# Optimization experiments

Measured on AMD Instinct MI355X. Metric: run time of the kernel, lower is better.

The kernel has to match this reference:

```python
import jax, jax.numpy as jnp
import numpy as np

N, E = 50000, 800000
DIN, DOUT, DEDGE, HEADS = 128, 128, 64, 1


def setup_inputs() -> dict:
    key = jax.random.key(0)
    ks = jax.random.split(key, 16)
    s = 0.02
    inp = {
        "x": jax.random.normal(ks[0], (N, DIN), jnp.float32),
        "edge_index": jax.random.randint(ks[1], (2, E), 0, N, dtype=jnp.int32),
        "edge_attr": jax.random.normal(ks[2], (E, DEDGE), jnp.float32),
        # TransformerConv params (PyG defaults: q/k/v/skip have bias, lin_edge has no bias)
        "Wq": jax.random.normal(ks[3], (DIN, HEADS * DOUT), jnp.float32) * s,
        "bq": jnp.zeros((HEADS * DOUT,), jnp.float32),
        "Wk": jax.random.normal(ks[4], (DIN, HEADS * DOUT), jnp.float32) * s,
        "bk": jnp.zeros((HEADS * DOUT,), jnp.float32),
        "Wv": jax.random.normal(ks[5], (DIN, HEADS * DOUT), jnp.float32) * s,
        "bv": jnp.zeros((HEADS * DOUT,), jnp.float32),
        "We": jax.random.normal(ks[6], (DEDGE, HEADS * DOUT), jnp.float32) * s,
        "Wskip": jax.random.normal(ks[7], (DIN, HEADS * DOUT), jnp.float32) * s,
        "bskip": jnp.zeros((HEADS * DOUT,), jnp.float32),
        # LayerNorm
        "ln_g": jnp.ones((DOUT,), jnp.float32),
        "ln_b": jnp.zeros((DOUT,), jnp.float32),
        # GatedResidualConnection
        "Wres": jax.random.normal(ks[8], (DIN, DOUT), jnp.float32) * s,
        "bres": jnp.zeros((DOUT,), jnp.float32),
        "Wgate": jax.random.normal(ks[9], (DIN, 1), jnp.float32) * s,
        "bgate": jnp.zeros((1,), jnp.float32),
    }
    return inp


def _transformer_conv(x, edge_index, edge_attr, Wq, bq, Wk, bk, Wv, bv, We, Wskip, bskip):
    H, C = HEADS, DOUT
    src, dst = edge_index[0], edge_index[1]  # j -> i (aggregate at dst)
    q = (x @ Wq + bq).reshape(-1, H, C)
    k = (x @ Wk + bk).reshape(-1, H, C)
    v = (x @ Wv + bv).reshape(-1, H, C)
    e = (edge_attr @ We).reshape(-1, H, C)  # [E,H,C]
    k_j = k[src] + e
    v_j = v[src] + e
    q_i = q[dst]
    alpha = jnp.sum(q_i * k_j, axis=-1) / jnp.sqrt(jnp.float32(C))  # [E,H]
    # segment softmax over incoming edges of each dst node
    amax = jax.ops.segment_max(alpha, dst, num_segments=N)  # [N,H]
    ex = jnp.exp(alpha - amax[dst])
    denom = jax.ops.segment_sum(ex, dst, num_segments=N)  # [N,H]
    p = ex / denom[dst]  # [E,H]
    out = jax.ops.segment_sum(p[..., None] * v_j, dst, num_segments=N)  # [N,H,C]
    out = out.reshape(-1, H * C)
    out = out + (x @ Wskip + bskip)  # root weight skip
    return out


def reference(x, edge_index, edge_attr, Wq, bq, Wk, bk, Wv, bv, We, Wskip, bskip,
              ln_g, ln_b, Wres, bres, Wgate, bgate):
    out = _transformer_conv(x, edge_index, edge_attr, Wq, bq, Wk, bk, Wv, bv, We, Wskip, bskip)
    # LayerNorm(out_channels)
    mu = jnp.mean(out, axis=-1, keepdims=True)
    var = jnp.mean(jnp.square(out - mu), axis=-1, keepdims=True)
    out = (out - mu) / jnp.sqrt(var + 1e-5) * ln_g + ln_b
    out = jax.nn.relu(out)
    # gated residual
    residual = x @ Wres + bres
    gate = jax.nn.sigmoid(x @ Wgate + bgate)  # [N,1]
    return gate * out + (1.0 - gate) * residual
```

## Files before the change

kernel.cpp:

```cpp
#include <hip/hip_runtime.h>
#include <math.h>

#define NN 50000
#define EE 800000
#define NPAD 50048
#define PC 768

typedef short bf16x8 __attribute__((ext_vector_type(8)));
typedef float f32x4 __attribute__((ext_vector_type(4)));

#define ASCALE 0.08838834764831845f

__device__ inline unsigned short f2bf(float f)
{
    unsigned u = __float_as_uint(f);
    u = u + 0x7fff + ((u >> 16) & 1);
    return (unsigned short)(u >> 16);
}

__global__ __launch_bounds__(256) void k_wprep(const float* __restrict__ Wq,
                                               const float* __restrict__ bq,
                                               const float* __restrict__ We,
                                               float* __restrict__ wqe,
                                               float* __restrict__ bqe)
{
    int idx = blockIdx.x * 256 + threadIdx.x;
    if (idx < 8192) {
        int r = idx >> 6, m = idx & 63;
        float acc = 0.f;
        for (int c = 0; c < 128; ++c) acc += Wq[r * 128 + c] * We[m * 128 + c];
        wqe[r * 64 + m] = acc;
    } else if (idx < 8256) {
        int m = idx - 8192;
        float acc = 0.f;
        for (int c = 0; c < 128; ++c) acc += bq[c] * We[m * 128 + c];
        bqe[m] = acc;
    }
}

__global__ __launch_bounds__(256) void k_packx(const float* __restrict__ x,
                                               short* __restrict__ Xb)
{
    int t = blockIdx.x * 256 + threadIdx.x;
    int base = t * 4;
    if (base >= NPAD * 128) return;
    short s0 = 0, s1 = 0, s2 = 0, s3 = 0;
    if (base < NN * 128) {
        const float4 v = *(const float4*)(x + base);
        s0 = f2bf(v.x); s1 = f2bf(v.y); s2 = f2bf(v.z); s3 = f2bf(v.w);
    }
    short4 o; o.x = s0; o.y = s1; o.z = s2; o.w = s3;
    *(short4*)(Xb + base) = o;
}

__global__ __launch_bounds__(256) void k_packw(
    const float* __restrict__ Wq, const float* __restrict__ bq,
    const float* __restrict__ Wk, const float* __restrict__ bk,
    const float* __restrict__ Wv, const float* __restrict__ bv,
    const float* __restrict__ Wskip, const float* __restrict__ bskip,
    const float* __restrict__ Wres, const float* __restrict__ bres,
    const float* __restrict__ Wgate, const float* __restrict__ bgate,
    const float* __restrict__ wqe, const float* __restrict__ bqe,
    const float* __restrict__ We,
    short* __restrict__ WT, float* __restrict__ bias,
    unsigned short* __restrict__ WeTb)
{
    int idx = blockIdx.x * 256 + threadIdx.x;
    if (idx < PC * 128) {
        int col = idx >> 7, k = idx & 127;
        float v;
        if (col < 128)      v = Wq[k * 128 + col];
        else if (col < 256) v = Wk[k * 128 + (col - 128)];
        else if (col < 384) v = Wv[k * 128 + (col - 256)];
        else if (col < 512) v = Wskip[k * 128 + (col - 384)];
        else if (col < 640) v = Wres[k * 128 + (col - 512)];
        else if (col < 704) v = wqe[k * 64 + (col - 640)];
        else if (col == 704) v = Wgate[k];
        else                v = 0.f;
        WT[col * 128 + k] = (short)f2bf(v);
    } else if (idx < PC * 128 + PC) {
        int col = idx - PC * 128;
        float b;
        if (col < 128)      b = bq[col];
        else if (col < 256) b = bk[col - 128];
        else if (col < 384) b = bv[col - 256];
        else if (col < 512) b = bskip[col - 384];
        else if (col < 640) b = bres[col - 512];
        else if (col < 704) b = bqe[col - 640];
        else if (col == 704) b = bgate[0];
        else                b = 0.f;
        bias[col] = b;
    } else if (idx < PC * 128 + PC + 128 * 72) {
        int i2 = idx - (PC * 128 + PC);
        int c = i2 / 72, kk = i2 % 72;
        WeTb[i2] = (kk < 64) ? f2bf(We[kk * 128 + c]) : (unsigned short)0;
    }
}

#define LROW 136
__global__ __launch_bounds__(256) void k_gemm(const short* __restrict__ Xb,
                                              const short* __restrict__ WT,
                                              const float* __restrict__ bias,
                                              float* __restrict__ P,
                                              unsigned short* __restrict__ KVb16)
{
    __shared__ short Al[128 * LROW];
    __shared__ short Bl[64 * LROW];

    int bn = blockIdx.x;
    int bm = blockIdx.y;
    int tid = threadIdx.x;

    const short* gA = Xb + (size_t)bm * 128 * 128;
    const short* gB = WT + (size_t)bn * 64 * 128;

#pragma unroll
    for (int it = 0; it < 8; ++it) {
        int g = it * 256 + tid;
        int row = g >> 4, c8 = g & 15;
        *(bf16x8*)&Al[row * LROW + c8 * 8] = *(const bf16x8*)(gA + g * 8);
    }
#pragma unroll
    for (int it = 0; it < 4; ++it) {
        int g = it * 256 + tid;
        int row = g >> 4, c8 = g & 15;
        *(bf16x8*)&Bl[row * LROW + c8 * 8] = *(const bf16x8*)(gB + g * 8);
    }
    __syncthreads();

    int wave = tid >> 6, lane = tid & 63;
    int quad = lane >> 4, l16 = lane & 15;
    int r0 = wave * 32;

    f32x4 acc[2][4] = {};
#pragma unroll
    for (int ks = 0; ks < 4; ++ks) {
        int k0 = ks * 32 + quad * 8;
        bf16x8 af0 = *(const bf16x8*)&Al[(r0 + l16) * LROW + k0];
        bf16x8 af1 = *(const bf16x8*)&Al[(r0 + 16 + l16) * LROW + k0];
#pragma unroll
        for (int cn = 0; cn < 4; ++cn) {
            bf16x8 bfr = *(const bf16x8*)&Bl[(cn * 16 + l16) * LROW + k0];
            acc[0][cn] = __builtin_amdgcn_mfma_f32_16x16x32_bf16(af0, bfr, acc[0][cn], 0, 0, 0);
            acc[1][cn] = __builtin_amdgcn_mfma_f32_16x16x32_bf16(af1, bfr, acc[1][cn], 0, 0, 0);
        }
    }

    bool isKV = (bn >= 2 && bn <= 5);
#pragma unroll
    for (int half = 0; half < 2; ++half) {
        int growb = bm * 128 + r0 + half * 16 + quad * 4;
#pragma unroll
        for (int cn = 0; cn < 4; ++cn) {
            int gcol = bn * 64 + cn * 16 + l16;
            float b = bias[gcol];
#pragma unroll
            for (int i = 0; i < 4; ++i) {
                int grow = growb + i;
                if (grow < NN) {
                    float v = acc[half][cn][i] + b;
                    if (isKV) {
                        int c, sub;
                        if (gcol < 192)      { c = gcol - 128; sub = 0; }
                        else if (gcol < 256) { c = gcol - 192; sub = 1; }
                        else if (gcol < 320) { c = gcol - 256; sub = 2; }
                        else                 { c = gcol - 320; sub = 3; }
                        KVb16[(size_t)grow * 256 + c * 4 + sub] = f2bf(v);
                    } else {
                        if (gcol == 704) v = 1.f / (1.f + __expf(-v));
                        P[(size_t)grow * PC + gcol] = v;
                    }
                }
            }
        }
    }
}

__global__ __launch_bounds__(256) void k_hist(const int* __restrict__ ei,
                                              int* __restrict__ deg, int E)
{
    int e = blockIdx.x * 256 + threadIdx.x;
    if (e < E) atomicAdd(&deg[ei[E + e]], 1);
}

__global__ __launch_bounds__(256) void k_scan1(const int* __restrict__ deg,
                                               int* __restrict__ rs,
                                               int* __restrict__ cs, int n)
{
    __shared__ int sh[256];
    int base = blockIdx.x * 1024;
    int t = threadIdx.x;
    int idx = base + t * 4;
    int v[4];
#pragma unroll
    for (int k = 0; k < 4; ++k) v[k] = (idx + k < n) ? deg[idx + k] : 0;
    int sum = v[0] + v[1] + v[2] + v[3];
    sh[t] = sum;
    __syncthreads();
    for (int off = 1; off < 256; off <<= 1) {
        int add = (t >= off) ? sh[t - off] : 0;
        __syncthreads();
        sh[t] += add;
        __syncthreads();
    }
    int run = sh[t] - sum;
    if (t == 255) cs[blockIdx.x] = sh[255];
#pragma unroll
    for (int k = 0; k < 4; ++k) {
        if (idx + k < n) rs[idx + k] = run;
        run += v[k];
    }
}

__global__ void k_scan2(int* __restrict__ cs, int nc)
{
    __shared__ int sh[64];
    int t = threadIdx.x;
    sh[t] = (t < nc) ? cs[t] : 0;
    __syncthreads();
    if (t == 0) {
        int acc = 0;
        for (int i = 0; i < nc; ++i) { int v = sh[i]; sh[i] = acc; acc += v; }
    }
    __syncthreads();
    if (t < nc) cs[t] = sh[t];
}

__global__ __launch_bounds__(256) void k_scan3(int* __restrict__ rs,
                                               const int* __restrict__ cs,
                                               int* __restrict__ cur, int n, int E)
{
    int i = blockIdx.x * 256 + threadIdx.x;
    if (i < n) {
        int v = rs[i] + cs[i >> 10];
        rs[i] = v;
        cur[i] = v;
    } else if (i == n) {
        rs[n] = E;
    }
}

__global__ __launch_bounds__(256) void k_scatter(const int* __restrict__ ei,
                                                 int* __restrict__ cur,
                                                 int2* __restrict__ sj, int E)
{
    int e = blockIdx.x * 256 + threadIdx.x;
    if (e < E) {
        int d = ei[E + e];
        int pos = atomicAdd(&cur[d], 1);
        int2 v; v.x = ei[e]; v.y = e;
        sj[pos] = v;
    }
}

__global__ __launch_bounds__(256) void k_attn_fused(
    const float* __restrict__ P, const unsigned int* __restrict__ KVb,
    const float* __restrict__ ea, const unsigned short* __restrict__ WeTb,
    const int* __restrict__ rs, const int2* __restrict__ sj,
    const float* __restrict__ ln_g, const float* __restrict__ ln_b,
    float* __restrict__ out)
{
    __shared__ unsigned short Sb_l[4 * 64];
    __shared__ float att_l[4 * 128];

    int tid = threadIdx.x;
    int wave = tid >> 6, lane = tid & 63;
    int node = blockIdx.x * 4 + wave;

    const float* Prow = P + (size_t)node * PC;
    float q0 = Prow[lane];
    float q1 = Prow[64 + lane];
    float wq = Prow[640 + lane];

    float accd = 0.f, t0 = 0.f, t1 = 0.f, sA = 0.f;
    int beg = rs[node], end = rs[node + 1];

    int p = beg;
    for (; p + 8 <= end; p += 8) {
        float pp[8], aa[8], v0[8], v1[8];
#pragma unroll
        for (int u = 0; u < 8; ++u) {
            long long sv = __builtin_nontemporal_load((const long long*)(sj + p + u));
            int sx = (int)sv, sy = (int)(sv >> 32);
            uint2 kv2 = *(const uint2*)(KVb + (size_t)sx * 128 + 2 * lane);
            float a = __builtin_nontemporal_load(ea + (size_t)sy * 64 + lane);
            float k0 = __uint_as_float(kv2.x << 16);
            float k1 = __uint_as_float(kv2.x & 0xffff0000u);
            v0[u] = __uint_as_float(kv2.y << 16);
            v1[u] = __uint_as_float(kv2.y & 0xffff0000u);
            aa[u] = a;
            pp[u] = q0 * k0 + q1 * k1 + wq * a;
        }
#pragma unroll
        for (int o = 32; o > 0; o >>= 1) {
#pragma unroll
            for (int u = 0; u < 8; ++u) pp[u] += __shfl_xor(pp[u], o);
        }
#pragma unroll
        for (int u = 0; u < 8; ++u) {
            float ex = __expf(pp[u] * ASCALE);
            accd += ex;
            t0 += ex * v0[u];
            t1 += ex * v1[u];
            sA += ex * aa[u];
        }
    }
    for (; p + 4 <= end; p += 4) {
        float pp[4], aa[4], v0[4], v1[4];
#pragma unroll
        for (int u = 0; u < 4; ++u) {
            long long sv = __builtin_nontemporal_load((const long long*)(sj + p + u));
            int sx = (int)sv, sy = (int)(sv >> 32);
            uint2 kv2 = *(const uint2*)(KVb + (size_t)sx * 128 + 2 * lane);
            float a = __builtin_nontemporal_load(ea + (size_t)sy * 64 + lane);
            float k0 = __uint_as_float(kv2.x << 16);
            float k1 = __uint_as_float(kv2.x & 0xffff0000u);
            v0[u] = __uint_as_float(kv2.y << 16);
            v1[u] = __uint_as_float(kv2.y & 0xffff0000u);
            aa[u] = a;
            pp[u] = q0 * k0 + q1 * k1 + wq * a;
        }
#pragma unroll
        for (int o = 32; o > 0; o >>= 1) {
#pragma unroll
            for (int u = 0; u < 4; ++u) pp[u] += __shfl_xor(pp[u], o);
        }
#pragma unroll
        for (int u = 0; u < 4; ++u) {
            float ex = __expf(pp[u] * ASCALE);
            accd += ex;
            t0 += ex * v0[u];
            t1 += ex * v1[u];
            sA += ex * aa[u];
        }
    }
    for (; p < end; ++p) {
        long long sv = __builtin_nontemporal_load((const long long*)(sj + p));
        int sx = (int)sv, sy = (int)(sv >> 32);
        uint2 kv2 = *(const uint2*)(KVb + (size_t)sx * 128 + 2 * lane);
        float a = __builtin_nontemporal_load(ea + (size_t)sy * 64 + lane);
        float k0 = __uint_as_float(kv2.x << 16);
        float k1 = __uint_as_float(kv2.x & 0xffff0000u);
        float vv0 = __uint_as_float(kv2.y << 16);
        float vv1 = __uint_as_float(kv2.y & 0xffff0000u);
        float part = q0 * k0 + q1 * k1 + wq * a;
#pragma unroll
        for (int o = 32; o > 0; o >>= 1) part += __shfl_xor(part, o);
        float ex = __expf(part * ASCALE);
        accd += ex;
        t0 += ex * vv0;
        t1 += ex * vv1;
        sA += ex * a;
    }


    Sb_l[wave * 64 + lane] = f2bf(sA);
    __syncthreads();

    {
        int quad = lane >> 4, l16 = lane & 15;
        int arow = l16 & 3;
        bf16x8 a0 = *(const bf16x8*)&Sb_l[arow * 64 + quad * 8];
        bf16x8 a1 = *(const bf16x8*)&Sb_l[arow * 64 + 32 + quad * 8];
#pragma unroll
        for (int c2 = 0; c2 < 2; ++c2) {
            int cn = wave * 2 + c2;
            int r = cn * 16 + l16;
            bf16x8 b0 = *(const bf16x8*)(WeTb + r * 72 + quad * 8);
            bf16x8 b1 = *(const bf16x8*)(WeTb + r * 72 + 32 + quad * 8);
            f32x4 acc = {};
            acc = __builtin_amdgcn_mfma_f32_16x16x32_bf16(a0, b0, acc, 0, 0, 0);
            acc = __builtin_amdgcn_mfma_f32_16x16x32_bf16(a1, b1, acc, 0, 0, 0);
            if (quad == 0) {
#pragma unroll
                for (int i = 0; i < 4; ++i)
                    att_l[i * 128 + cn * 16 + l16] = acc[i];
            }
        }
    }
    __syncthreads();

    float rcp = accd > 0.f ? 1.f / accd : 0.f;
    float a0f = (t0 + att_l[wave * 128 + lane]) * rcp + Prow[384 + lane];
    float a1f = (t1 + att_l[wave * 128 + 64 + lane]) * rcp + Prow[448 + lane];

    float s = a0f + a1f;
#pragma unroll
    for (int o = 32; o > 0; o >>= 1) s += __shfl_xor(s, o);
    float mean = s * (1.f / 128.f);
    float d0 = a0f - mean, d1 = a1f - mean;
    float vs = d0 * d0 + d1 * d1;
#pragma unroll
    for (int o = 32; o > 0; o >>= 1) vs += __shfl_xor(vs, o);
    float inv = rsqrtf(vs * (1.f / 128.f) + 1e-5f);
    float n0 = d0 * inv * ln_g[lane] + ln_b[lane];
    float n1 = d1 * inv * ln_g[64 + lane] + ln_b[64 + lane];
    n0 = fmaxf(n0, 0.f);
    n1 = fmaxf(n1, 0.f);

    float g = Prow[704];
    float r0 = Prow[512 + lane];
    float r1 = Prow[576 + lane];
    out[(size_t)node * 128 + lane] = g * n0 + (1.f - g) * r0;
    out[(size_t)node * 128 + 64 + lane] = g * n1 + (1.f - g) * r1;
}

extern "C" void kernel_launch(void* const* d_in, const int* in_sizes, int n_in,
                              void* d_out, int out_size, void* d_ws, size_t ws_size,
                              hipStream_t stream)
{
    const float* x     = (const float*)d_in[0];
    const int*   ei    = (const int*)d_in[1];
    const float* ea    = (const float*)d_in[2];
    const float* Wq    = (const float*)d_in[3];
    const float* bq    = (const float*)d_in[4];
    const float* Wk    = (const float*)d_in[5];
    const float* bk    = (const float*)d_in[6];
    const float* Wv    = (const float*)d_in[7];
    const float* bv    = (const float*)d_in[8];
    const float* We    = (const float*)d_in[9];
    const float* Wskip = (const float*)d_in[10];
    const float* bskip = (const float*)d_in[11];
    const float* ln_g  = (const float*)d_in[12];
    const float* ln_b  = (const float*)d_in[13];
    const float* Wres  = (const float*)d_in[14];
    const float* bres  = (const float*)d_in[15];
    const float* Wgate = (const float*)d_in[16];
    const float* bgate = (const float*)d_in[17];
    float* out = (float*)d_out;

    float* W = (float*)d_ws;
    size_t o = 0;
    auto falloc = [&](size_t e) { size_t r = o; o += e; return r; };
    size_t oP    = falloc((size_t)NN * PC);
    size_t oWQE  = falloc(8192);
    size_t oBQE  = falloc(64);
    size_t oBIAS = falloc(PC);
    size_t oKVB  = falloc((size_t)NN * 128);

    short* SB = (short*)(W + o);
    size_t oXB  = 0;
    size_t oWT  = oXB + (size_t)NPAD * 128;
    size_t oWET = oWT + (size_t)PC * 128;
    size_t sh_total = oWET + 128 * 72;

    int* IB = (int*)(SB + ((sh_total + 1) & ~(size_t)1));
    size_t io = 0;
    auto ialloc = [&](size_t e) { size_t r = io; io += e; return r; };
    size_t oSJ   = ialloc((size_t)2 * EE);
    size_t oDEG  = ialloc(NN);
    size_t oRS   = ialloc(NN + 1);
    size_t oCUR  = ialloc(NN);
    size_t oCS   = ialloc(64);

    hipMemsetAsync(IB + oDEG, 0, NN * sizeof(int), stream);

    k_wprep<<<33, 256, 0, stream>>>(Wq, bq, We, W + oWQE, W + oBQE);
    k_packx<<<(NPAD * 128 / 4 + 255) / 256, 256, 0, stream>>>(x, SB + oXB);
    k_packw<<<(PC * 128 + PC + 128 * 72 + 255) / 256, 256, 0, stream>>>(
        Wq, bq, Wk, bk, Wv, bv, Wskip, bskip, Wres, bres, Wgate, bgate,
        W + oWQE, W + oBQE, We, SB + oWT, W + oBIAS,
        (unsigned short*)(SB + oWET));

    dim3 ggrid(PC / 64, NPAD / 128);
    k_gemm<<<ggrid, 256, 0, stream>>>(SB + oXB, SB + oWT, W + oBIAS, W + oP,
                                      (unsigned short*)(W + oKVB));

    k_hist<<<(EE + 255) / 256, 256, 0, stream>>>(ei, IB + oDEG, EE);
    k_scan1<<<49, 256, 0, stream>>>(IB + oDEG, IB + oRS, IB + oCS, NN);
    k_scan2<<<1, 64, 0, stream>>>(IB + oCS, 49);
    k_scan3<<<(NN + 256) / 256, 256, 0, stream>>>(IB + oRS, IB + oCS, IB + oCUR, NN, EE);
    k_scatter<<<(EE + 255) / 256, 256, 0, stream>>>(ei, IB + oCUR, (int2*)(IB + oSJ), EE);

    k_attn_fused<<<NN / 4, 256, 0, stream>>>(
        W + oP, (const unsigned int*)(W + oKVB), ea,
        (const unsigned short*)(SB + oWET),
        IB + oRS, (const int2*)(IB + oSJ), ln_g, ln_b, out);
}
```

Baseline: 565.3 us.

## Store skip/residual/gate projections in bf16 and schedule nodes by degree

The GEMM output is split into an fp32 query buffer and a bf16 buffer holding the skip, residual, qe and gate columns, which shrinks the per-node projection traffic written by the GEMM and read by the attention kernel. A counting sort by in-degree (histogram, scan, scatter) builds a node permutation so the waves in a block handle nodes with similar degree, reducing load imbalance inside blocks. This adds three small kernels, and the bf16 rounding of the skip and residual terms slightly lowers precision.

```diff
diff --git a/kernel.cpp b/kernel.cpp
--- a/kernel.cpp
+++ b/kernel.cpp
@@ -16,6 +16,11 @@
     unsigned u = __float_as_uint(f);
     u = u + 0x7fff + ((u >> 16) & 1);
     return (unsigned short)(u >> 16);
+}
+
+__device__ inline float bfu(unsigned short us)
+{
+    return __uint_as_float((unsigned)us << 16);
 }
 
 __global__ __launch_bounds__(256) void k_wprep(const float* __restrict__ Wq,
@@ -101,7 +106,8 @@
 __global__ __launch_bounds__(256) void k_gemm(const short* __restrict__ Xb,
                                               const short* __restrict__ WT,
                                               const float* __restrict__ bias,
-                                              float* __restrict__ P,
+                                              float* __restrict__ Pq,
+                                              unsigned short* __restrict__ Pe,
                                               unsigned short* __restrict__ KVb16)
 {
     __shared__ short Al[128 * LROW];
@@ -159,16 +165,18 @@
                 int grow = growb + i;
                 if (grow < NN) {
                     float v = acc[half][cn][i] + b;
-                    if (isKV) {
+                    if (bn < 2) {
+                        Pq[(size_t)grow * 128 + gcol] = v;
+                    } else if (isKV) {
                         int c, sub;
                         if (gcol < 192)      { c = gcol - 128; sub = 0; }
                         else if (gcol < 256) { c = gcol - 192; sub = 1; }
                         else if (gcol < 320) { c = gcol - 256; sub = 2; }
                         else                 { c = gcol - 320; sub = 3; }
                         KVb16[(size_t)grow * 256 + c * 4 + sub] = f2bf(v);
-                    } else {
+                    } else if (gcol <= 704) {
                         if (gcol == 704) v = 1.f / (1.f + __expf(-v));
-                        P[(size_t)grow * PC + gcol] = v;
+                        Pe[(size_t)grow * 384 + (gcol - 384)] = f2bf(v);
                     }
                 }
             }
@@ -253,10 +261,48 @@
     }
 }
 
+__global__ __launch_bounds__(256) void k_dhist(const int* __restrict__ deg,
+                                               int* __restrict__ dcnt)
+{
+    int i = blockIdx.x * 256 + threadIdx.x;
+    if (i < NN) {
+        int d = deg[i]; if (d > 63) d = 63;
+        atomicAdd(&dcnt[d], 1);
+    }
+}
+
+__global__ void k_dscan(const int* __restrict__ dcnt, int* __restrict__ dcur)
+{
+    __shared__ int sh[64];
+    int t = threadIdx.x;
+    sh[t] = dcnt[t];
+    __syncthreads();
+    if (t == 0) {
+        int acc = 0;
+        for (int d = 63; d >= 0; --d) { int v = sh[d]; sh[d] = acc; acc += v; }
+    }
+    __syncthreads();
+    dcur[t] = sh[t];
+}
+
+__global__ __launch_bounds__(256) void k_dscatter(const int* __restrict__ deg,
+                                                  int* __restrict__ dcur,
+                                                  int* __restrict__ perm)
+{
+    int i = blockIdx.x * 256 + threadIdx.x;
+    if (i < NN) {
+        int d = deg[i]; if (d > 63) d = 63;
+        int pos = atomicAdd(&dcur[d], 1);
+        perm[pos] = i;
+    }
+}
+
 __global__ __launch_bounds__(256) void k_attn_fused(
-    const float* __restrict__ P, const unsigned int* __restrict__ KVb,
+    const float* __restrict__ Pq, const unsigned short* __restrict__ Pe,
+    const unsigned int* __restrict__ KVb,
     const float* __restrict__ ea, const unsigned short* __restrict__ WeTb,
     const int* __restrict__ rs, const int2* __restrict__ sj,
+    const int* __restrict__ perm,
     const float* __restrict__ ln_g, const float* __restrict__ ln_b,
     float* __restrict__ out)
 {
@@ -265,12 +311,13 @@
 
     int tid = threadIdx.x;
     int wave = tid >> 6, lane = tid & 63;
-    int node = blockIdx.x * 4 + wave;
-
-    const float* Prow = P + (size_t)node * PC;
-    float q0 = Prow[lane];
-    float q1 = Prow[64 + lane];
-    float wq = Prow[640 + lane];
+    int node = perm[blockIdx.x * 4 + wave];
+
+    const float* Qrow = Pq + (size_t)node * 128;
+    const unsigned short* Erow = Pe + (size_t)node * 384;
+    float q0 = Qrow[lane];
+    float q1 = Qrow[64 + lane];
+    float wq = bfu(Erow[256 + lane]);
 
     float accd = 0.f, t0 = 0.f, t1 = 0.f, sA = 0.f;
     int beg = rs[node], end = rs[node + 1];
@@ -381,8 +428,8 @@
     __syncthreads();
 
     float rcp = accd > 0.f ? 1.f / accd : 0.f;
-    float a0f = (t0 + att_l[wave * 128 + lane]) * rcp + Prow[384 + lane];
-    float a1f = (t1 + att_l[wave * 128 + 64 + lane]) * rcp + Prow[448 + lane];
+    float a0f = (t0 + att_l[wave * 128 + lane]) * rcp + bfu(Erow[lane]);
+    float a1f = (t1 + att_l[wave * 128 + 64 + lane]) * rcp + bfu(Erow[64 + lane]);
 
     float s = a0f + a1f;
 #pragma unroll
@@ -398,9 +445,9 @@
     n0 = fmaxf(n0, 0.f);
     n1 = fmaxf(n1, 0.f);
 
-    float g = Prow[704];
-    float r0 = Prow[512 + lane];
-    float r1 = Prow[576 + lane];
+    float g = bfu(Erow[320]);
+    float r0 = bfu(Erow[128 + lane]);
+    float r1 = bfu(Erow[192 + lane]);
     out[(size_t)node * 128 + lane] = g * n0 + (1.f - g) * r0;
     out[(size_t)node * 128 + 64 + lane] = g * n1 + (1.f - g) * r1;
 }
@@ -432,7 +479,7 @@
     float* W = (float*)d_ws;
     size_t o = 0;
     auto falloc = [&](size_t e) { size_t r = o; o += e; return r; };
-    size_t oP    = falloc((size_t)NN * PC);
+    size_t oPQ   = falloc((size_t)NN * 128);
     size_t oWQE  = falloc(8192);
     size_t oBQE  = falloc(64);
     size_t oBIAS = falloc(PC);
@@ -442,18 +489,22 @@
     size_t oXB  = 0;
     size_t oWT  = oXB + (size_t)NPAD * 128;
     size_t oWET = oWT + (size_t)PC * 128;
-    size_t sh_total = oWET + 128 * 72;
+    size_t oPE  = oWET + 128 * 72;
+    size_t sh_total = oPE + (size_t)NN * 384;
 
     int* IB = (int*)(SB + ((sh_total + 1) & ~(size_t)1));
     size_t io = 0;
     auto ialloc = [&](size_t e) { size_t r = io; io += e; return r; };
     size_t oSJ   = ialloc((size_t)2 * EE);
     size_t oDEG  = ialloc(NN);
+    size_t oDCNT = ialloc(64);
     size_t oRS   = ialloc(NN + 1);
     size_t oCUR  = ialloc(NN);
     size_t oCS   = ialloc(64);
-
-    hipMemsetAsync(IB + oDEG, 0, NN * sizeof(int), stream);
+    size_t oDCUR = ialloc(64);
+    size_t oPERM = ialloc(NN);
+
+    hipMemsetAsync(IB + oDEG, 0, (NN + 64) * sizeof(int), stream);
 
     k_wprep<<<33, 256, 0, stream>>>(Wq, bq, We, W + oWQE, W + oBQE);
     k_packx<<<(NPAD * 128 / 4 + 255) / 256, 256, 0, stream>>>(x, SB + oXB);
@@ -463,17 +514,22 @@
         (unsigned short*)(SB + oWET));
 
     dim3 ggrid(PC / 64, NPAD / 128);
-    k_gemm<<<ggrid, 256, 0, stream>>>(SB + oXB, SB + oWT, W + oBIAS, W + oP,
+    k_gemm<<<ggrid, 256, 0, stream>>>(SB + oXB, SB + oWT, W + oBIAS, W + oPQ,
+                                      (unsigned short*)(SB + oPE),
                                       (unsigned short*)(W + oKVB));
 
     k_hist<<<(EE + 255) / 256, 256, 0, stream>>>(ei, IB + oDEG, EE);
+    k_dhist<<<(NN + 255) / 256, 256, 0, stream>>>(IB + oDEG, IB + oDCNT);
     k_scan1<<<49, 256, 0, stream>>>(IB + oDEG, IB + oRS, IB + oCS, NN);
     k_scan2<<<1, 64, 0, stream>>>(IB + oCS, 49);
     k_scan3<<<(NN + 256) / 256, 256, 0, stream>>>(IB + oRS, IB + oCS, IB + oCUR, NN, EE);
+    k_dscan<<<1, 64, 0, stream>>>(IB + oDCNT, IB + oDCUR);
     k_scatter<<<(EE + 255) / 256, 256, 0, stream>>>(ei, IB + oCUR, (int2*)(IB + oSJ), EE);
+    k_dscatter<<<(NN + 255) / 256, 256, 0, stream>>>(IB + oDEG, IB + oDCUR, IB + oPERM);
 
     k_attn_fused<<<NN / 4, 256, 0, stream>>>(
-        W + oP, (const unsigned int*)(W + oKVB), ea,
+        W + oPQ, (const unsigned short*)(SB + oPE),
+        (const unsigned int*)(W + oKVB), ea,
         (const unsigned short*)(SB + oWET),
-        IB + oRS, (const int2*)(IB + oSJ), ln_g, ln_b, out);
-}
+        IB + oRS, (const int2*)(IB + oSJ), IB + oPERM, ln_g, ln_b, out);
+}
```

Result: slower. 795.2 us (+40.7%).
